# Kernel tuning notes

Measured on AMD Instinct MI355X. Metric: run time of the kernel, lower is better.

Reference implementation:

```python
import jax, jax.numpy as jnp
import numpy as np

MAX_DIST = 8
GUIDANCE_WEIGHT = 0.4
EPS_MAG = 1e-6
EPS_COS = 1e-8
EPS_WSUM = 1e-8


def setup_inputs() -> dict:
    key = jax.random.key(0)
    k1, k2 = jax.random.split(key)
    embeddings = jax.random.normal(k1, (4, 2048, 1024), dtype=jnp.float32)
    guidance_trajectories = jax.random.normal(k2, (512, 1024), dtype=jnp.float32)
    return {"embeddings": embeddings, "guidance_trajectories": guidance_trajectories}


def reference(embeddings, guidance_trajectories):
    B, S, D = embeddings.shape
    W = min(MAX_DIST, S - 1)  # fixed max window size

    # consecutive-token trajectory vectors: diffs[t] = emb[t+1] - emb[t]
    diffs = embeddings[:, 1:, :] - embeddings[:, :-1, :]          # [B, S-1, D]

    # sliding windows of the last W diffs ending at pos-1
    pos = jnp.arange(S)[:, None]                                  # [S, 1]
    k = jnp.arange(W)[None, :]                                    # [1, W]
    idx = pos - W + k                                             # diff index per slot
    valid = (idx >= 0) & (pos >= 1)                               # [S, W]
    windows = diffs[:, jnp.clip(idx, 0, S - 2), :]                # [B, S, W, D]

    # torch.linspace(0.1, 1.0, w) weights, per-position window size w = min(pos, W);
    # valid entries occupy the last w slots of the W-wide window.
    w = jnp.minimum(pos, W)                                       # [S, 1]
    j = k - (W - w)                                               # local index within window
    lin = jnp.where(w > 1, 0.1 + 0.9 * j / jnp.maximum(w - 1, 1), 0.1)
    pos_weights = jnp.where(valid, lin, 0.0).astype(embeddings.dtype)  # [S, W]

    # normalize trajectory vectors, zero where magnitude <= 1e-6
    mag = jnp.linalg.norm(windows, axis=-1, keepdims=True)        # [B, S, W, 1]
    is_valid_mag = mag > EPS_MAG
    normed = jnp.where(is_valid_mag, windows / jnp.where(is_valid_mag, mag, 1.0), 0.0)

    mag_weights = jnp.tanh(mag * 2.0)                             # [B, S, W, 1]
    combined = pos_weights[None, :, :, None] * mag_weights        # [B, S, W, 1]

    # guidance influence: softmax over cosine similarity to guidance bank
    g_norm = jnp.linalg.norm(guidance_trajectories, axis=-1)      # [G]
    a_norm = jnp.linalg.norm(normed, axis=-1)                     # [B, S, W]
    dots = jnp.einsum('bswd,gd->bswg', normed, guidance_trajectories)
    sims = dots / (jnp.maximum(a_norm, EPS_COS)[..., None] * jnp.maximum(g_norm, EPS_COS))
    g_weights = jax.nn.softmax(sims * 2.0, axis=-1)               # [B, S, W, G]
    influence = jnp.einsum('bswg,gd->bswd', g_weights, guidance_trajectories)
    blended = (1.0 - GUIDANCE_WEIGHT) * normed + GUIDANCE_WEIGHT * influence

    weight_sum = jnp.maximum(combined.sum(axis=2), EPS_WSUM)      # [B, S, 1]
    trajectories = (blended * combined).sum(axis=2) / weight_sum  # [B, S, D]
    return trajectories
```

## Files before the change

kernel.cpp:

```cpp
#include <hip/hip_runtime.h>
#include <math.h>

#define B_ 4
#define S_ 2048
#define D_ 1024
#define G_ 512
#define T_ 2047
#define R_ 8188
#define RPAD 8192
#define MT 16
#define ABST 1032

typedef __attribute__((ext_vector_type(8))) short short8;
typedef __attribute__((ext_vector_type(4))) short s16x4;
typedef __attribute__((ext_vector_type(4))) float f32x4;

#define WSOFF_RG2  0u
#define WSOFF_MAGW 2048u
#define WSOFF_BP1  34816u
#define WSOFF_BP2  1083392u
#define WSOFF_NH   2131968u
#define WSOFF_IH   18909184u

__device__ inline short to_bf16(float f) {
    union { float f; unsigned u; } v; v.f = f;
    unsigned r = v.u + 0x7fffu + ((v.u >> 16) & 1u);
    return (short)(r >> 16);
}
__device__ inline float fb(unsigned short h) {
    union { unsigned u; float f; } v;
    v.u = ((unsigned)h) << 16;
    return v.f;
}

__global__ __launch_bounds__(256) void prep_kernel(const float* __restrict__ guid,
                                                   float* __restrict__ rg2,
                                                   short8* __restrict__ Bp1,
                                                   short8* __restrict__ Bp2) {
    int bid = blockIdx.x, tid = threadIdx.x;
    if (bid < 128) {
        int wave = tid >> 6, lane = tid & 63;
        int g = bid * 4 + wave;
        const float4* gp = (const float4*)(guid + (size_t)g * D_);
        float ss = 0.f;
#pragma unroll
        for (int i = 0; i < 4; ++i) {
            float4 v = gp[lane + 64 * i];
            ss += v.x * v.x + v.y * v.y + v.z * v.z + v.w * v.w;
        }
#pragma unroll
        for (int m = 32; m >= 1; m >>= 1) ss += __shfl_xor(ss, m, 64);
        if (lane == 0) rg2[g] = 2.0f / fmaxf(sqrtf(ss), 1e-8f);
#pragma unroll
        for (int h = 0; h < 2; ++h) {
            int kg = lane + 64 * h;
            const float* src = guid + (size_t)g * D_ + kg * 8;
            short8 v;
#pragma unroll
            for (int j = 0; j < 8; ++j) v[j] = to_bf16(src[j]);
            Bp1[(size_t)kg * G_ + g] = v;
        }
    } else {
        int gg = bid - 128;
#pragma unroll
        for (int dd = 0; dd < 4; ++dd) {
            int d = tid + 256 * dd;
            short8 v;
#pragma unroll
            for (int j = 0; j < 8; ++j) v[j] = to_bf16(guid[(size_t)(gg * 8 + j) * D_ + d]);
            Bp2[(size_t)gg * D_ + d] = v;
        }
    }
}

__global__ __launch_bounds__(1024, 8) void fused_kernel(const float* __restrict__ emb,
                                                        const short8* __restrict__ Bp1,
                                                        const short8* __restrict__ Bp2,
                                                        const float* __restrict__ rg2,
                                                        float* __restrict__ magw,
                                                        short* __restrict__ normh,
                                                        short* __restrict__ inflh) {
    __shared__ short AB[MT][ABST];
    __shared__ float rg2s[G_];
    __shared__ float pred[MT][16];
    __shared__ float redmx[MT], redrs[MT];

    const int tid = threadIdx.x;
    const int wave = tid >> 6, lane = tid & 63;
    const int l15 = lane & 15, quad = lane >> 4;
    const int r0 = blockIdx.x * MT;

    if (tid < G_) rg2s[tid] = rg2[tid];

    {
        int rr = wave;
        int R = r0 + rr;
        if (R < R_) {
            int b = R / T_;
            int t = R - b * T_;
            const float4* p = (const float4*)(emb + ((size_t)b * S_ + t) * D_);
            float4 dv[4]; float ss = 0.f;
#pragma unroll
            for (int j = 0; j < 4; ++j) {
                float4 x0 = p[lane + 64 * j];
                float4 x1 = p[lane + 64 * j + 256];
                dv[j] = make_float4(x1.x - x0.x, x1.y - x0.y, x1.z - x0.z, x1.w - x0.w);
                ss += dv[j].x * dv[j].x + dv[j].y * dv[j].y + dv[j].z * dv[j].z + dv[j].w * dv[j].w;
            }
#pragma unroll
            for (int m = 32; m >= 1; m >>= 1) ss += __shfl_xor(ss, m, 64);
            float mag = sqrtf(ss);
            float rmag = (mag > 1e-6f) ? (1.0f / mag) : 0.0f;
            if (lane == 0) magw[R] = tanhf(2.0f * mag);
            short* nb = normh + (size_t)R * D_ + 4 * lane;
#pragma unroll
            for (int j = 0; j < 4; ++j) {
                s16x4 h;
                h[0] = to_bf16(dv[j].x * rmag); h[1] = to_bf16(dv[j].y * rmag);
                h[2] = to_bf16(dv[j].z * rmag); h[3] = to_bf16(dv[j].w * rmag);
                *(s16x4*)(nb + 256 * j) = h;
                *(s16x4*)&AB[rr][4 * lane + 256 * j] = h;
            }
        } else {
            s16x4 z = (s16x4)0;
#pragma unroll
            for (int j = 0; j < 4; ++j) *(s16x4*)&AB[rr][4 * lane + 256 * j] = z;
        }
    }
    __syncthreads();

    f32x4 acc1[2];
    acc1[0] = (f32x4)0.f; acc1[1] = (f32x4)0.f;
    {
        const short8* Bb = Bp1 + (size_t)quad * G_ + wave * 32 + l15;
        short8 bc0 = Bb[0], bc1 = Bb[16], bn0, bn1;
        for (int ks = 0; ks < 32; ++ks) {
            if (ks < 31) {
                const short8* Bx = Bb + (size_t)(ks + 1) * 4 * G_;
                bn0 = Bx[0]; bn1 = Bx[16];
            }
            short8 a0 = *(const short8*)&AB[l15][ks * 32 + quad * 8];
            acc1[0] = __builtin_amdgcn_mfma_f32_16x16x32_bf16(a0, bc0, acc1[0], 0, 0, 0);
            acc1[1] = __builtin_amdgcn_mfma_f32_16x16x32_bf16(a0, bc1, acc1[1], 0, 0, 0);
            bc0 = bn0; bc1 = bn1;
        }
    }

    {
        float pmax[4];
#pragma unroll
        for (int r2 = 0; r2 < 4; ++r2) pmax[r2] = -1e30f;
#pragma unroll
        for (int nt = 0; nt < 2; ++nt) {
            float rgv = rg2s[wave * 32 + nt * 16 + l15];
#pragma unroll
            for (int r2 = 0; r2 < 4; ++r2) {
                float lg = acc1[nt][r2] * rgv;
                acc1[nt][r2] = lg;
                pmax[r2] = fmaxf(pmax[r2], lg);
            }
        }
#pragma unroll
        for (int m = 8; m >= 1; m >>= 1)
#pragma unroll
            for (int r2 = 0; r2 < 4; ++r2)
                pmax[r2] = fmaxf(pmax[r2], __shfl_xor(pmax[r2], m, 16));
        if (l15 == 0) {
#pragma unroll
            for (int r2 = 0; r2 < 4; ++r2)
                pred[quad * 4 + r2][wave] = pmax[r2];
        }
        __syncthreads();
        if (tid < MT) {
            float m = pred[tid][0];
#pragma unroll
            for (int w2 = 1; w2 < 16; ++w2) m = fmaxf(m, pred[tid][w2]);
            redmx[tid] = m;
        }
        __syncthreads();
        float psum[4];
#pragma unroll
        for (int r2 = 0; r2 < 4; ++r2) psum[r2] = 0.f;
#pragma unroll
        for (int nt = 0; nt < 2; ++nt)
#pragma unroll
            for (int r2 = 0; r2 < 4; ++r2) {
                float e = __expf(acc1[nt][r2] - redmx[quad * 4 + r2]);
                acc1[nt][r2] = e;
                psum[r2] += e;
            }
#pragma unroll
        for (int m = 8; m >= 1; m >>= 1)
#pragma unroll
            for (int r2 = 0; r2 < 4; ++r2)
                psum[r2] += __shfl_xor(psum[r2], m, 16);
        if (l15 == 0) {
#pragma unroll
            for (int r2 = 0; r2 < 4; ++r2)
                pred[quad * 4 + r2][wave] = psum[r2];
        }
        __syncthreads();
        if (tid < MT) {
            float s = 0.f;
#pragma unroll
            for (int w2 = 0; w2 < 16; ++w2) s += pred[tid][w2];
            redrs[tid] = 1.0f / s;
        }
        __syncthreads();
#pragma unroll
        for (int nt = 0; nt < 2; ++nt)
#pragma unroll
            for (int r2 = 0; r2 < 4; ++r2) {
                int row = quad * 4 + r2;
                AB[row][wave * 32 + nt * 16 + l15] =
                    to_bf16(acc1[nt][r2] * redrs[row]);
            }
    }
    __syncthreads();

    f32x4 acc2[4];
#pragma unroll
    for (int nt = 0; nt < 4; ++nt) acc2[nt] = (f32x4)0.f;
#pragma unroll
    for (int half = 0; half < 2; ++half) {
        const short8* Bb = Bp2 + (size_t)quad * D_ + wave * 64 + half * 32 + l15;
        short8 bc0 = Bb[0], bc1 = Bb[16], bn0, bn1;
        for (int ks = 0; ks < 16; ++ks) {
            if (ks < 15) {
                const short8* Bx = Bb + (size_t)(ks + 1) * 4 * D_;
                bn0 = Bx[0]; bn1 = Bx[16];
            }
            short8 a0 = *(const short8*)&AB[l15][ks * 32 + quad * 8];
            acc2[half * 2 + 0] = __builtin_amdgcn_mfma_f32_16x16x32_bf16(a0, bc0, acc2[half * 2 + 0], 0, 0, 0);
            acc2[half * 2 + 1] = __builtin_amdgcn_mfma_f32_16x16x32_bf16(a0, bc1, acc2[half * 2 + 1], 0, 0, 0);
            bc0 = bn0; bc1 = bn1;
        }
    }

#pragma unroll
    for (int half = 0; half < 2; ++half)
#pragma unroll
        for (int ntl = 0; ntl < 2; ++ntl) {
            int d = wave * 64 + half * 32 + ntl * 16 + l15;
#pragma unroll
            for (int r2 = 0; r2 < 4; ++r2) {
                int R = r0 + quad * 4 + r2;
                if (R < R_) inflh[(size_t)R * D_ + d] = to_bf16(acc2[half * 2 + ntl][r2]);
            }
        }
}

__global__ __launch_bounds__(256) void combine_kernel(const float* __restrict__ magw,
                                                      const unsigned short* __restrict__ normh,
                                                      const unsigned short* __restrict__ inflh,
                                                      float* __restrict__ out) {
    int blk = blockIdx.x;
    int b = blk >> 8;
    int rem = blk & 255;
    int s0 = (rem >> 1) * 16;
    int d = (rem & 1) * 512 + threadIdx.x * 2;
    size_t rbase = (size_t)b * T_;

    float2 ring[8]; float mring[8];
#pragma unroll
    for (int a2 = 0; a2 < 8; ++a2) { ring[a2] = make_float2(0.f, 0.f); mring[a2] = 0.f; }

#define LOADBL(t_, dst_)                                                        \
    {                                                                           \
        size_t off_ = (rbase + (t_)) * D_ + d;                                  \
        ushort2 n2_ = *(const ushort2*)(normh + off_);                          \
        ushort2 i2_ = *(const ushort2*)(inflh + off_);                          \
        dst_ = make_float2(0.6f * fb(n2_.x) + 0.4f * fb(i2_.x),                 \
                           0.6f * fb(n2_.y) + 0.4f * fb(i2_.y));                \
    }

#pragma unroll
    for (int a2 = 0; a2 < 7; ++a2) {
        int t = s0 - 8 + a2;
        if (t >= 0) {
            LOADBL(t, ring[a2]);
            mring[a2] = magw[rbase + t];
        }
    }
    if (s0 != 0) {
#pragma unroll
        for (int i = 0; i < 16; ++i) {
            int t = s0 + i - 1;
            LOADBL(t, ring[(i + 7) & 7]);
            mring[(i + 7) & 7] = magw[rbase + t];
            float2 acc = make_float2(0.f, 0.f); float wsum = 0.f;
#pragma unroll
            for (int a = 1; a <= 8; ++a) {
                int slot = (i - a) & 7;
                float lin = 0.1f + (0.9f / 7.0f) * (float)(8 - a);
                float wt = lin * mring[slot];
                acc.x += wt * ring[slot].x; acc.y += wt * ring[slot].y;
                wsum += wt;
            }
            float rws = 1.0f / fmaxf(wsum, 1e-8f);
            *(float2*)&out[((size_t)b * S_ + s0 + i) * D_ + d] =
                make_float2(acc.x * rws, acc.y * rws);
        }
    } else {
#pragma unroll
        for (int i = 0; i < 16; ++i) {
            if (i >= 1) {
                int t = i - 1;
                LOADBL(t, ring[(i + 7) & 7]);
                mring[(i + 7) & 7] = magw[rbase + t];
            }
            int w = (i < 8) ? i : 8;
            float rw = (w > 1) ? 0.9f / (float)(w - 1) : 0.0f;
            float2 acc = make_float2(0.f, 0.f); float wsum = 0.f;
            for (int a = 1; a <= w; ++a) {
                int slot = (i - a) & 7;
                float lin = 0.1f + rw * (float)(w - a);
                float wt = lin * mring[slot];
                acc.x += wt * ring[slot].x; acc.y += wt * ring[slot].y;
                wsum += wt;
            }
            float rws = 1.0f / fmaxf(wsum, 1e-8f);
            *(float2*)&out[((size_t)b * S_ + i) * D_ + d] =
                make_float2(acc.x * rws, acc.y * rws);
        }
    }
#undef LOADBL
}

extern "C" void kernel_launch(void* const* d_in, const int* in_sizes, int n_in,
                              void* d_out, int out_size, void* d_ws, size_t ws_size,
                              hipStream_t stream) {
    const float* emb  = (const float*)d_in[0];
    const float* guid = (const float*)d_in[1];
    float* out = (float*)d_out;
    char* ws = (char*)d_ws;

    float*  rg2   = (float*)(ws + WSOFF_RG2);
    float*  magw  = (float*)(ws + WSOFF_MAGW);
    short8* Bp1   = (short8*)(ws + WSOFF_BP1);
    short8* Bp2   = (short8*)(ws + WSOFF_BP2);
    short*  normh = (short*)(ws + WSOFF_NH);
    short*  inflh = (short*)(ws + WSOFF_IH);

    prep_kernel<<<192, 256, 0, stream>>>(guid, rg2, Bp1, Bp2);
    fused_kernel<<<RPAD / MT, 1024, 0, stream>>>(emb, Bp1, Bp2, rg2, magw, normh, inflh);
    combine_kernel<<<B_ * 128 * 2, 256, 0, stream>>>(magw, (const unsigned short*)normh,
                                                     (const unsigned short*)inflh, out);
}
```

Before: 139.1 us.

## Fuse combine into main kernel, apply window weighting before second GEMM

Merges the combine pass into the fused kernel. Each block now handles 32 output positions plus an 8-row halo (48 diff rows), so normalized diffs and influence rows no longer round-trip through global bf16 buffers. The window weighting is applied to the softmax probabilities before the second GEMM, which cuts that GEMM from 8188 diff rows to 8192 output rows' worth of 32-row tiles, and the softmax max-subtraction is dropped since cosine logits are bounded. In exchange there is redundant halo work (48 rows computed per 32 outputs), only 256 large blocks, heavier LDS use, and raw barriers.

```diff
diff --git a/kernel.cpp b/kernel.cpp
--- a/kernel.cpp
+++ b/kernel.cpp
@@ -6,21 +6,18 @@
 #define D_ 1024
 #define G_ 512
 #define T_ 2047
-#define R_ 8188
-#define RPAD 8192
-#define MT 16
-#define ABST 1032
+#define MTO 32
+#define NR 48
+#define ABST2 1032
+#define VST 520
 
 typedef __attribute__((ext_vector_type(8))) short short8;
 typedef __attribute__((ext_vector_type(4))) short s16x4;
 typedef __attribute__((ext_vector_type(4))) float f32x4;
 
-#define WSOFF_RG2  0u
-#define WSOFF_MAGW 2048u
-#define WSOFF_BP1  34816u
-#define WSOFF_BP2  1083392u
-#define WSOFF_NH   2131968u
-#define WSOFF_IH   18909184u
+#define WSOFF_RG2 0u
+#define WSOFF_BP1 4096u
+#define WSOFF_BP2 (4096u + 1048576u)
 
 __device__ inline short to_bf16(float f) {
     union { float f; unsigned u; } v; v.f = f;
@@ -32,6 +29,17 @@
     v.u = ((unsigned)h) << 16;
     return v.f;
 }
+__device__ inline float fbs(short h) { return fb((unsigned short)h); }
+__device__ inline f32x4 MF(short8 a, short8 b, f32x4 c) {
+    return __builtin_amdgcn_mfma_f32_16x16x32_bf16(a, b, c, 0, 0, 0);
+}
+
+#define RAWBAR() do {                                            \
+    __builtin_amdgcn_sched_barrier(0);                           \
+    asm volatile("s_waitcnt lgkmcnt(0)" ::: "memory");           \
+    __builtin_amdgcn_s_barrier();                                \
+    __builtin_amdgcn_sched_barrier(0);                           \
+} while (0)
 
 __global__ __launch_bounds__(256) void prep_kernel(const float* __restrict__ guid,
                                                    float* __restrict__ rg2,
@@ -73,258 +81,263 @@
     }
 }
 
-__global__ __launch_bounds__(1024, 8) void fused_kernel(const float* __restrict__ emb,
+#define G1Q3(ksv, q)  {                                                           \
+    short8 a0 = *(const short8*)&ABs[l15][(ksv) * 32 + quad * 8];                 \
+    short8 a1 = *(const short8*)&ABs[16 + l15][(ksv) * 32 + quad * 8];            \
+    short8 a2 = *(const short8*)&ABs[32 + l15][(ksv) * 32 + quad * 8];            \
+    acc1[0][0] = MF(a0, q[0], acc1[0][0]); acc1[0][1] = MF(a0, q[1], acc1[0][1]); \
+    acc1[1][0] = MF(a1, q[0], acc1[1][0]); acc1[1][1] = MF(a1, q[1], acc1[1][1]); \
+    acc1[2][0] = MF(a2, q[0], acc1[2][0]); acc1[2][1] = MF(a2, q[1], acc1[2][1]); }
+
+__global__ __launch_bounds__(1024, 4) void fused_kernel(const float* __restrict__ emb,
                                                         const short8* __restrict__ Bp1,
                                                         const short8* __restrict__ Bp2,
                                                         const float* __restrict__ rg2,
-                                                        float* __restrict__ magw,
-                                                        short* __restrict__ normh,
-                                                        short* __restrict__ inflh) {
-    __shared__ short AB[MT][ABST];
+                                                        float* __restrict__ out) {
+    __shared__ short ABs[NR][ABST2];
+    __shared__ short Vs[MTO][VST];
     __shared__ float rg2s[G_];
-    __shared__ float pred[MT][16];
-    __shared__ float redmx[MT], redrs[MT];
+    __shared__ float pred[NR][16];
+    __shared__ float magS[NR], rmagS[NR], mrS[NR], cvS[NR];
+    __shared__ float rwsS[MTO];
 
     const int tid = threadIdx.x;
     const int wave = tid >> 6, lane = tid & 63;
     const int l15 = lane & 15, quad = lane >> 4;
-    const int r0 = blockIdx.x * MT;
+    const int bid = blockIdx.x;
+    const int b = bid >> 6;
+    const int s0 = (bid & 63) << 5;
+    const bool edge = (s0 == 0);
 
     if (tid < G_) rg2s[tid] = rg2[tid];
 
-    {
-        int rr = wave;
-        int R = r0 + rr;
-        if (R < R_) {
-            int b = R / T_;
-            int t = R - b * T_;
+#pragma unroll
+    for (int ii = 0; ii < 3; ++ii) {
+        int rr = wave + 16 * ii;
+        int t = s0 - 8 + rr;
+        bool valid = (t >= 0) && (rr < 39);
+        float ss = 0.f;
+        if (valid) {
             const float4* p = (const float4*)(emb + ((size_t)b * S_ + t) * D_);
-            float4 dv[4]; float ss = 0.f;
 #pragma unroll
             for (int j = 0; j < 4; ++j) {
                 float4 x0 = p[lane + 64 * j];
                 float4 x1 = p[lane + 64 * j + 256];
-                dv[j] = make_float4(x1.x - x0.x, x1.y - x0.y, x1.z - x0.z, x1.w - x0.w);
-                ss += dv[j].x * dv[j].x + dv[j].y * dv[j].y + dv[j].z * dv[j].z + dv[j].w * dv[j].w;
-            }
-#pragma unroll
-            for (int m = 32; m >= 1; m >>= 1) ss += __shfl_xor(ss, m, 64);
-            float mag = sqrtf(ss);
-            float rmag = (mag > 1e-6f) ? (1.0f / mag) : 0.0f;
-            if (lane == 0) magw[R] = tanhf(2.0f * mag);
-            short* nb = normh + (size_t)R * D_ + 4 * lane;
-#pragma unroll
-            for (int j = 0; j < 4; ++j) {
+                float4 dv = make_float4(x1.x - x0.x, x1.y - x0.y, x1.z - x0.z, x1.w - x0.w);
+                ss += dv.x * dv.x + dv.y * dv.y + dv.z * dv.z + dv.w * dv.w;
                 s16x4 h;
-                h[0] = to_bf16(dv[j].x * rmag); h[1] = to_bf16(dv[j].y * rmag);
-                h[2] = to_bf16(dv[j].z * rmag); h[3] = to_bf16(dv[j].w * rmag);
-                *(s16x4*)(nb + 256 * j) = h;
-                *(s16x4*)&AB[rr][4 * lane + 256 * j] = h;
+                h[0] = to_bf16(dv.x); h[1] = to_bf16(dv.y);
+                h[2] = to_bf16(dv.z); h[3] = to_bf16(dv.w);
+                *(s16x4*)&ABs[rr][4 * lane + 256 * j] = h;
             }
         } else {
             s16x4 z = (s16x4)0;
 #pragma unroll
-            for (int j = 0; j < 4; ++j) *(s16x4*)&AB[rr][4 * lane + 256 * j] = z;
-        }
-    }
-    __syncthreads();
-
-    f32x4 acc1[2];
-    acc1[0] = (f32x4)0.f; acc1[1] = (f32x4)0.f;
+            for (int j = 0; j < 4; ++j) *(s16x4*)&ABs[rr][4 * lane + 256 * j] = z;
+        }
+#pragma unroll
+        for (int m = 32; m >= 1; m >>= 1) ss += __shfl_xor(ss, m, 64);
+        float mag = sqrtf(ss);
+        if (lane == 0) {
+            magS[rr]  = tanhf(2.0f * mag);
+            rmagS[rr] = (mag > 1e-6f) ? (1.0f / mag) : 0.0f;
+        }
+    }
+    RAWBAR();
+
+    if (tid < NR) mrS[tid] = 0.6f * magS[tid] * rmagS[tid];
+    if (tid < MTO) {
+        int w = edge ? ((tid < 8) ? tid : 8) : 8;
+        float rw = (w > 1) ? 0.9f / (float)(w - 1) : 0.f;
+        float s = 0.f;
+#pragma unroll
+        for (int a = 1; a <= 8; ++a) {
+            float lin = (a <= w) ? ((w > 1) ? (0.1f + rw * (float)(w - a)) : 0.1f) : 0.f;
+            s += lin * magS[tid + 8 - a];
+        }
+        rwsS[tid] = 1.0f / fmaxf(s, 1e-8f);
+    }
+
+    f32x4 acc1[3][2];
+#pragma unroll
+    for (int mt = 0; mt < 3; ++mt)
+#pragma unroll
+        for (int nt = 0; nt < 2; ++nt) acc1[mt][nt] = (f32x4)0.f;
     {
         const short8* Bb = Bp1 + (size_t)quad * G_ + wave * 32 + l15;
-        short8 bc0 = Bb[0], bc1 = Bb[16], bn0, bn1;
-        for (int ks = 0; ks < 32; ++ks) {
-            if (ks < 31) {
-                const short8* Bx = Bb + (size_t)(ks + 1) * 4 * G_;
-                bn0 = Bx[0]; bn1 = Bx[16];
-            }
-            short8 a0 = *(const short8*)&AB[l15][ks * 32 + quad * 8];
-            acc1[0] = __builtin_amdgcn_mfma_f32_16x16x32_bf16(a0, bc0, acc1[0], 0, 0, 0);
-            acc1[1] = __builtin_amdgcn_mfma_f32_16x16x32_bf16(a0, bc1, acc1[1], 0, 0, 0);
-            bc0 = bn0; bc1 = bn1;
-        }
-    }
-
+        short8 q0[2], q1[2], q2[2], q3[2];
+        q0[0] = Bb[0];          q0[1] = Bb[16];
+        q1[0] = Bb[4 * G_];     q1[1] = Bb[4 * G_ + 16];
+        q2[0] = Bb[8 * G_];     q2[1] = Bb[8 * G_ + 16];
+        q3[0] = Bb[12 * G_];    q3[1] = Bb[12 * G_ + 16];
+#pragma unroll
+        for (int k4 = 0; k4 < 32; k4 += 4) {
+            G1Q3(k4 + 0, q0); if (k4 < 28) { q0[0] = Bb[(size_t)(k4 + 4) * 4 * G_]; q0[1] = Bb[(size_t)(k4 + 4) * 4 * G_ + 16]; }
+            G1Q3(k4 + 1, q1); if (k4 < 28) { q1[0] = Bb[(size_t)(k4 + 5) * 4 * G_]; q1[1] = Bb[(size_t)(k4 + 5) * 4 * G_ + 16]; }
+            G1Q3(k4 + 2, q2); if (k4 < 28) { q2[0] = Bb[(size_t)(k4 + 6) * 4 * G_]; q2[1] = Bb[(size_t)(k4 + 6) * 4 * G_ + 16]; }
+            G1Q3(k4 + 3, q3); if (k4 < 28) { q3[0] = Bb[(size_t)(k4 + 7) * 4 * G_]; q3[1] = Bb[(size_t)(k4 + 7) * 4 * G_ + 16]; }
+        }
+    }
+    RAWBAR();
+
+    float np_[MTO];
     {
-        float pmax[4];
-#pragma unroll
-        for (int r2 = 0; r2 < 4; ++r2) pmax[r2] = -1e30f;
-#pragma unroll
-        for (int nt = 0; nt < 2; ++nt) {
-            float rgv = rg2s[wave * 32 + nt * 16 + l15];
-#pragma unroll
-            for (int r2 = 0; r2 < 4; ++r2) {
-                float lg = acc1[nt][r2] * rgv;
-                acc1[nt][r2] = lg;
-                pmax[r2] = fmaxf(pmax[r2], lg);
-            }
-        }
+        float pr[8];
+#pragma unroll
+        for (int r = 0; r < 8; ++r) pr[r] = mrS[r] * fbs(ABs[r][tid]);
+        if (!edge) {
+#pragma unroll
+            for (int i = 0; i < MTO; ++i) {
+                float s = 0.f;
+#pragma unroll
+                for (int a = 1; a <= 8; ++a)
+                    s += (0.1f + (0.9f / 7.f) * (float)(8 - a)) * pr[(i + 8 - a) & 7];
+                np_[i] = s;
+                if (i < 31) pr[i & 7] = mrS[i + 8] * fbs(ABs[i + 8][tid]);
+            }
+        } else {
+#pragma unroll
+            for (int i = 0; i < MTO; ++i) {
+                int w = (i < 8) ? i : 8;
+                float rw = (w > 1) ? 0.9f / (float)(w - 1) : 0.f;
+                float s = 0.f;
+#pragma unroll
+                for (int a = 1; a <= 8; ++a) {
+                    float lin = (a <= w) ? ((w > 1) ? (0.1f + rw * (float)(w - a)) : 0.1f) : 0.f;
+                    s += lin * pr[(i + 8 - a) & 7];
+                }
+                np_[i] = s;
+                if (i < 31) pr[i & 7] = mrS[i + 8] * fbs(ABs[i + 8][tid]);
+            }
+        }
+    }
+
+    float psum[3][4];
+#pragma unroll
+    for (int mt = 0; mt < 3; ++mt)
+#pragma unroll
+        for (int r2 = 0; r2 < 4; ++r2) psum[mt][r2] = 0.f;
+    {
+        float rmv[3][4];
+#pragma unroll
+        for (int mt = 0; mt < 3; ++mt)
+#pragma unroll
+            for (int r2 = 0; r2 < 4; ++r2) rmv[mt][r2] = rmagS[mt * 16 + quad * 4 + r2];
+#pragma unroll
+        for (int mt = 0; mt < 3; ++mt)
+#pragma unroll
+            for (int nt = 0; nt < 2; ++nt) {
+                float rgv = rg2s[wave * 32 + nt * 16 + l15];
+#pragma unroll
+                for (int r2 = 0; r2 < 4; ++r2) {
+                    float e = __expf(acc1[mt][nt][r2] * rgv * rmv[mt][r2]);
+                    acc1[mt][nt][r2] = e;
+                    psum[mt][r2] += e;
+                }
+            }
 #pragma unroll
         for (int m = 8; m >= 1; m >>= 1)
 #pragma unroll
+            for (int mt = 0; mt < 3; ++mt)
+#pragma unroll
+                for (int r2 = 0; r2 < 4; ++r2)
+                    psum[mt][r2] += __shfl_xor(psum[mt][r2], m, 16);
+    }
+    RAWBAR();
+#pragma unroll
+    for (int mt = 0; mt < 3; ++mt)
+#pragma unroll
+        for (int nt = 0; nt < 2; ++nt)
+#pragma unroll
             for (int r2 = 0; r2 < 4; ++r2)
-                pmax[r2] = fmaxf(pmax[r2], __shfl_xor(pmax[r2], m, 16));
-        if (l15 == 0) {
+                ABs[mt * 16 + quad * 4 + r2][wave * 32 + nt * 16 + l15] =
+                    to_bf16(acc1[mt][nt][r2]);
+    if (l15 == 0) {
+#pragma unroll
+        for (int mt = 0; mt < 3; ++mt)
 #pragma unroll
             for (int r2 = 0; r2 < 4; ++r2)
-                pred[quad * 4 + r2][wave] = pmax[r2];
-        }
-        __syncthreads();
-        if (tid < MT) {
-            float m = pred[tid][0];
-#pragma unroll
-            for (int w2 = 1; w2 < 16; ++w2) m = fmaxf(m, pred[tid][w2]);
-            redmx[tid] = m;
-        }
-        __syncthreads();
-        float psum[4];
-#pragma unroll
-        for (int r2 = 0; r2 < 4; ++r2) psum[r2] = 0.f;
-#pragma unroll
-        for (int nt = 0; nt < 2; ++nt)
-#pragma unroll
-            for (int r2 = 0; r2 < 4; ++r2) {
-                float e = __expf(acc1[nt][r2] - redmx[quad * 4 + r2]);
-                acc1[nt][r2] = e;
-                psum[r2] += e;
-            }
-#pragma unroll
-        for (int m = 8; m >= 1; m >>= 1)
-#pragma unroll
-            for (int r2 = 0; r2 < 4; ++r2)
-                psum[r2] += __shfl_xor(psum[r2], m, 16);
-        if (l15 == 0) {
-#pragma unroll
-            for (int r2 = 0; r2 < 4; ++r2)
-                pred[quad * 4 + r2][wave] = psum[r2];
-        }
-        __syncthreads();
-        if (tid < MT) {
-            float s = 0.f;
-#pragma unroll
-            for (int w2 = 0; w2 < 16; ++w2) s += pred[tid][w2];
-            redrs[tid] = 1.0f / s;
-        }
-        __syncthreads();
-#pragma unroll
-        for (int nt = 0; nt < 2; ++nt)
-#pragma unroll
-            for (int r2 = 0; r2 < 4; ++r2) {
-                int row = quad * 4 + r2;
-                AB[row][wave * 32 + nt * 16 + l15] =
-                    to_bf16(acc1[nt][r2] * redrs[row]);
-            }
-    }
-    __syncthreads();
-
-    f32x4 acc2[4];
-#pragma unroll
-    for (int nt = 0; nt < 4; ++nt) acc2[nt] = (f32x4)0.f;
+                pred[mt * 16 + quad * 4 + r2][wave] = psum[mt][r2];
+    }
+    RAWBAR();
+    if (tid < NR) {
+        float s = 0.f;
+#pragma unroll
+        for (int w2 = 0; w2 < 16; ++w2) s += pred[tid][w2];
+        cvS[tid] = 0.4f * magS[tid] / s;
+    }
+    RAWBAR();
+
+#pragma unroll
+    for (int ii = 0; ii < 2; ++ii) {
+        int i = wave * 2 + ii;
+        int w = edge ? ((i < 8) ? i : 8) : 8;
+        float rw = (w > 1) ? 0.9f / (float)(w - 1) : 0.f;
+        float c[8];
+#pragma unroll
+        for (int a = 1; a <= 8; ++a) {
+            float lin = (a <= w) ? ((w > 1) ? (0.1f + rw * (float)(w - a)) : 0.1f) : 0.f;
+            c[a - 1] = lin * cvS[i + 8 - a];
+        }
+        float v[8];
+#pragma unroll
+        for (int j = 0; j < 8; ++j) v[j] = 0.f;
+#pragma unroll
+        for (int a = 1; a <= 8; ++a) {
+            short8 e = *(const short8*)&ABs[i + 8 - a][lane * 8];
+#pragma unroll
+            for (int j = 0; j < 8; ++j) v[j] += c[a - 1] * fbs(e[j]);
+        }
+        short8 vo;
+#pragma unroll
+        for (int j = 0; j < 8; ++j) vo[j] = to_bf16(v[j]);
+        *(short8*)&Vs[i][lane * 8] = vo;
+    }
+    RAWBAR();
+
+    short* IPb = &ABs[0][0];
 #pragma unroll
     for (int half = 0; half < 2; ++half) {
-        const short8* Bb = Bp2 + (size_t)quad * D_ + wave * 64 + half * 32 + l15;
-        short8 bc0 = Bb[0], bc1 = Bb[16], bn0, bn1;
+        f32x4 acc2[2][2];
+#pragma unroll
+        for (int mt = 0; mt < 2; ++mt)
+#pragma unroll
+            for (int nt = 0; nt < 2; ++nt) acc2[mt][nt] = (f32x4)0.f;
+        const short8* Bb2 = Bp2 + (size_t)quad * D_ + wave * 64 + half * 32 + l15;
+        short8 bc0 = Bb2[0], bc1 = Bb2[16], bn0, bn1;
+#pragma unroll
         for (int ks = 0; ks < 16; ++ks) {
             if (ks < 15) {
-                const short8* Bx = Bb + (size_t)(ks + 1) * 4 * D_;
+                const short8* Bx = Bb2 + (size_t)(ks + 1) * 4 * D_;
                 bn0 = Bx[0]; bn1 = Bx[16];
             }
-            short8 a0 = *(const short8*)&AB[l15][ks * 32 + quad * 8];
-            acc2[half * 2 + 0] = __builtin_amdgcn_mfma_f32_16x16x32_bf16(a0, bc0, acc2[half * 2 + 0], 0, 0, 0);
-            acc2[half * 2 + 1] = __builtin_amdgcn_mfma_f32_16x16x32_bf16(a0, bc1, acc2[half * 2 + 1], 0, 0, 0);
+            short8 a0 = *(const short8*)&Vs[l15][ks * 32 + quad * 8];
+            short8 a1 = *(const short8*)&Vs[16 + l15][ks * 32 + quad * 8];
+            acc2[0][0] = MF(a0, bc0, acc2[0][0]); acc2[0][1] = MF(a0, bc1, acc2[0][1]);
+            acc2[1][0] = MF(a1, bc0, acc2[1][0]); acc2[1][1] = MF(a1, bc1, acc2[1][1]);
             bc0 = bn0; bc1 = bn1;
         }
-    }
-
-#pragma unroll
-    for (int half = 0; half < 2; ++half)
-#pragma unroll
-        for (int ntl = 0; ntl < 2; ++ntl) {
-            int d = wave * 64 + half * 32 + ntl * 16 + l15;
-#pragma unroll
-            for (int r2 = 0; r2 < 4; ++r2) {
-                int R = r0 + quad * 4 + r2;
-                if (R < R_) inflh[(size_t)R * D_ + d] = to_bf16(acc2[half * 2 + ntl][r2]);
-            }
-        }
-}
-
-__global__ __launch_bounds__(256) void combine_kernel(const float* __restrict__ magw,
-                                                      const unsigned short* __restrict__ normh,
-                                                      const unsigned short* __restrict__ inflh,
-                                                      float* __restrict__ out) {
-    int blk = blockIdx.x;
-    int b = blk >> 8;
-    int rem = blk & 255;
-    int s0 = (rem >> 1) * 16;
-    int d = (rem & 1) * 512 + threadIdx.x * 2;
-    size_t rbase = (size_t)b * T_;
-
-    float2 ring[8]; float mring[8];
-#pragma unroll
-    for (int a2 = 0; a2 < 8; ++a2) { ring[a2] = make_float2(0.f, 0.f); mring[a2] = 0.f; }
-
-#define LOADBL(t_, dst_)                                                        \
-    {                                                                           \
-        size_t off_ = (rbase + (t_)) * D_ + d;                                  \
-        ushort2 n2_ = *(const ushort2*)(normh + off_);                          \
-        ushort2 i2_ = *(const ushort2*)(inflh + off_);                          \
-        dst_ = make_float2(0.6f * fb(n2_.x) + 0.4f * fb(i2_.x),                 \
-                           0.6f * fb(n2_.y) + 0.4f * fb(i2_.y));                \
-    }
-
-#pragma unroll
-    for (int a2 = 0; a2 < 7; ++a2) {
-        int t = s0 - 8 + a2;
-        if (t >= 0) {
-            LOADBL(t, ring[a2]);
-            mring[a2] = magw[rbase + t];
-        }
-    }
-    if (s0 != 0) {
-#pragma unroll
-        for (int i = 0; i < 16; ++i) {
-            int t = s0 + i - 1;
-            LOADBL(t, ring[(i + 7) & 7]);
-            mring[(i + 7) & 7] = magw[rbase + t];
-            float2 acc = make_float2(0.f, 0.f); float wsum = 0.f;
-#pragma unroll
-            for (int a = 1; a <= 8; ++a) {
-                int slot = (i - a) & 7;
-                float lin = 0.1f + (0.9f / 7.0f) * (float)(8 - a);
-                float wt = lin * mring[slot];
-                acc.x += wt * ring[slot].x; acc.y += wt * ring[slot].y;
-                wsum += wt;
-            }
-            float rws = 1.0f / fmaxf(wsum, 1e-8f);
-            *(float2*)&out[((size_t)b * S_ + s0 + i) * D_ + d] =
-                make_float2(acc.x * rws, acc.y * rws);
-        }
-    } else {
-#pragma unroll
-        for (int i = 0; i < 16; ++i) {
-            if (i >= 1) {
-                int t = i - 1;
-                LOADBL(t, ring[(i + 7) & 7]);
-                mring[(i + 7) & 7] = magw[rbase + t];
-            }
-            int w = (i < 8) ? i : 8;
-            float rw = (w > 1) ? 0.9f / (float)(w - 1) : 0.0f;
-            float2 acc = make_float2(0.f, 0.f); float wsum = 0.f;
-            for (int a = 1; a <= w; ++a) {
-                int slot = (i - a) & 7;
-                float lin = 0.1f + rw * (float)(w - a);
-                float wt = lin * mring[slot];
-                acc.x += wt * ring[slot].x; acc.y += wt * ring[slot].y;
-                wsum += wt;
-            }
-            float rws = 1.0f / fmaxf(wsum, 1e-8f);
-            *(float2*)&out[((size_t)b * S_ + i) * D_ + d] =
-                make_float2(acc.x * rws, acc.y * rws);
-        }
-    }
-#undef LOADBL
+#pragma unroll
+        for (int mt = 0; mt < 2; ++mt)
+#pragma unroll
+            for (int ntl = 0; ntl < 2; ++ntl) {
+                int d2 = wave * 64 + half * 32 + ntl * 16 + l15;
+#pragma unroll
+                for (int r2 = 0; r2 < 4; ++r2)
+                    IPb[(size_t)(mt * 16 + quad * 4 + r2) * ABST2 + d2] =
+                        to_bf16(acc2[mt][ntl][r2]);
+            }
+    }
+    RAWBAR();
+
+    {
+        float* ob = out + ((size_t)b * S_ + s0) * D_ + tid;
+#pragma unroll
+        for (int i = 0; i < MTO; ++i) {
+            float ip = fbs(IPb[(size_t)i * ABST2 + tid]);
+            ob[(size_t)i * D_] = (np_[i] + ip) * rwsS[i];
+        }
+    }
 }
 
 extern "C" void kernel_launch(void* const* d_in, const int* in_sizes, int n_in,
@@ -335,15 +348,10 @@
     float* out = (float*)d_out;
     char* ws = (char*)d_ws;
 
-    float*  rg2   = (float*)(ws + WSOFF_RG2);
-    float*  magw  = (float*)(ws + WSOFF_MAGW);
-    short8* Bp1   = (short8*)(ws + WSOFF_BP1);
-    short8* Bp2   = (short8*)(ws + WSOFF_BP2);
-    short*  normh = (short*)(ws + WSOFF_NH);
-    short*  inflh = (short*)(ws + WSOFF_IH);
+    float*  rg2 = (float*)(ws + WSOFF_RG2);
+    short8* Bp1 = (short8*)(ws + WSOFF_BP1);
+    short8* Bp2 = (short8*)(ws + WSOFF_BP2);
 
     prep_kernel<<<192, 256, 0, stream>>>(guid, rg2, Bp1, Bp2);
-    fused_kernel<<<RPAD / MT, 1024, 0, stream>>>(emb, Bp1, Bp2, rg2, magw, normh, inflh);
-    combine_kernel<<<B_ * 128 * 2, 256, 0, stream>>>(magw, (const unsigned short*)normh,
-                                                     (const unsigned short*)inflh, out);
-}
+    fused_kernel<<<256, 1024, 0, stream>>>(emb, Bp1, Bp2, rg2, out);
+}
```

New measurement: 121.1 us. -13.0%, faster.
